# Optimization experiments

Measured on AMD Instinct MI355X. Metric: run time of the kernel, lower is better.

## Reference

```python
import jax, jax.numpy as jnp
import numpy as np


def setup_inputs() -> dict:
    key = jax.random.key(0)
    ks = jax.random.split(key, 5)
    B, S, D = 2, 2048, 1024
    x = jax.random.normal(ks[0], (B, S, D), dtype=jnp.float32)
    # nn.Linear default init scale ~ 1/sqrt(fan_in); use scaled normals
    W_qkv = jax.random.normal(ks[1], (3 * D, D), dtype=jnp.float32) * (1.0 / np.sqrt(D))
    b_qkv = jax.random.normal(ks[2], (3 * D,), dtype=jnp.float32) * 0.01
    W_out = jax.random.normal(ks[3], (D, D), dtype=jnp.float32) * (1.0 / np.sqrt(D))
    b_out = jax.random.normal(ks[4], (D,), dtype=jnp.float32) * 0.01
    return {"x": x, "W_qkv": W_qkv, "b_qkv": b_qkv, "W_out": W_out, "b_out": b_out, "n_heads": 16}


def reference(x, W_qkv, b_qkv, W_out, b_out, n_heads):
    B, S, D = x.shape
    H = n_heads
    c = D // H
    scale = jnp.asarray(1.0 / np.sqrt(c), dtype=x.dtype)
    # qkv projection; torch layout: (head, qkv, c) along the 3*D output dim
    qkv = (x @ W_qkv.T + b_qkv).reshape(B, S, H, 3, c)
    q = qkv[..., 0, :]  # (B, S, H, c)
    k = qkv[..., 1, :]
    v = qkv[..., 2, :]
    scores = jnp.einsum("bshd,bthd->bhst", q, k) * scale  # (B, H, S, S)
    # mask='right': forbid attending to future positions (col > row)
    causal = jnp.arange(S)[None, :] > jnp.arange(S)[:, None]  # (S, S) True where future
    scores = jnp.where(causal[None, None], -jnp.inf, scores)
    attn = jax.nn.softmax(scores, axis=-1)
    ctx = jnp.einsum("bhst,bthd->bshd", attn, v).reshape(B, S, D)
    return ctx @ W_out.T + b_out
```

## Files before the change

kernel.cpp:

```cpp
#include <hip/hip_runtime.h>
#include <stdint.h>

#define B_ 2
#define S_ 2048
#define D_ 1024
#define H_ 16
#define C_ 64
#define M_ (B_*S_)
#define N1_ (3*D_)

typedef float f32x4 __attribute__((ext_vector_type(4)));
typedef float f32x16 __attribute__((ext_vector_type(16)));
typedef __bf16 bf16x8 __attribute__((ext_vector_type(8)));

#define QSCALE 0.18033688f

static __device__ __forceinline__ unsigned short f2bf(float f) {
  __bf16 h = (__bf16)f;
  return __builtin_bit_cast(unsigned short, h);
}
static __device__ __forceinline__ unsigned pk2(float lo, float hi) {
  return (unsigned)f2bf(lo) | ((unsigned)f2bf(hi) << 16);
}

static __device__ __forceinline__ f32x4 mfma_bf16(uint4 a, uint4 b, f32x4 c) {
  return __builtin_amdgcn_mfma_f32_16x16x32_bf16(
      __builtin_bit_cast(bf16x8, a), __builtin_bit_cast(bf16x8, b), c, 0, 0, 0);
}
static __device__ __forceinline__ f32x16 mfma32(uint4 a, uint4 b, f32x16 c) {
  return __builtin_amdgcn_mfma_f32_32x32x16_bf16(
      __builtin_bit_cast(bf16x8, a), __builtin_bit_cast(bf16x8, b), c, 0, 0, 0);
}

static __device__ __forceinline__ float xsum32(float x) {
  return x + __shfl_xor(x, 32);
}

static __device__ __forceinline__ void gload16(const void* g, void* l) {
  __builtin_amdgcn_global_load_lds(
      (const __attribute__((address_space(1))) unsigned int*)g,
      (__attribute__((address_space(3))) unsigned int*)l, 16, 0, 0);
}

#define N8X (M_*D_/8)
#define N8W (N1_*D_/8)
#define N8O (D_*D_/8)
__global__ __launch_bounds__(256) void cast_all(
    const float* __restrict__ x,   unsigned short* __restrict__ xb,
    const float* __restrict__ wq,  unsigned short* __restrict__ wqb,
    const float* __restrict__ wo,  unsigned short* __restrict__ wob) {
  int i = blockIdx.x * 256 + threadIdx.x;
  const float* src; unsigned short* dst; int j;
  if (i < N8X)              { src = x;  dst = xb;  j = i; }
  else if (i < N8X + N8W)   { src = wq; dst = wqb; j = i - N8X; }
  else                      { src = wo; dst = wob; j = i - N8X - N8W; }
  const float4* s4 = (const float4*)src;
  float4 a = s4[2*j], b = s4[2*j+1];
  uint4 o;
  o.x = pk2(a.x, a.y);
  o.y = pk2(a.z, a.w);
  o.z = pk2(b.x, b.y);
  o.w = pk2(b.z, b.w);
  ((uint4*)dst)[j] = o;
}

template<int MODE>
__global__ __launch_bounds__(256) void gemm_bt(
    const unsigned short* __restrict__ A,
    const unsigned short* __restrict__ Bm,
    const float* __restrict__ bias,
    float* __restrict__ Cf,
    unsigned short* __restrict__ Qg,
    unsigned short* __restrict__ Kf,
    unsigned short* __restrict__ Vf,
    int Ndim, int Kdim)
{
  __shared__ __attribute__((aligned(16))) unsigned short As[128*64];
  __shared__ __attribute__((aligned(16))) unsigned short Bs[128*64];
  const int tid = threadIdx.x;
  const int l = tid & 63, wid = tid >> 6;
  const int g = l >> 4, lr = l & 15;
  const int m0 = blockIdx.y * 128, n0 = blockIdx.x * 128;
  const int wr = (wid >> 1) * 64, wc = (wid & 1) * 64;

  f32x4 acc[4][4] = {};

  const int srow8 = l >> 3;
  const int schunk = (l & 7) ^ srow8;
  const unsigned short* Agl = A + (size_t)(m0 + wid*32 + srow8) * Kdim + schunk*8;
  const unsigned short* Bgl = Bm + (size_t)(n0 + wid*32 + srow8) * Kdim + schunk*8;
  unsigned short* Adst = &As[(wid*32)*64];
  unsigned short* Bdst = &Bs[(wid*32)*64];
  const size_t rstep = (size_t)8 * Kdim;

  for (int k0 = 0; k0 < Kdim; k0 += 64) {
    __syncthreads();
#pragma unroll
    for (int i = 0; i < 4; ++i) {
      gload16(Agl + k0 + i*rstep, Adst + i*8*64);
      gload16(Bgl + k0 + i*rstep, Bdst + i*8*64);
    }
    __syncthreads();
#pragma unroll
    for (int kk = 0; kk < 2; ++kk) {
      const int c = kk*4 + g;
      uint4 af[4], bf[4];
#pragma unroll
      for (int mi = 0; mi < 4; ++mi)
        af[mi] = *(const uint4*)&As[(wr + mi*16 + lr)*64 + ((c ^ (lr & 7))*8)];
#pragma unroll
      for (int ni = 0; ni < 4; ++ni)
        bf[ni] = *(const uint4*)&Bs[(wc + ni*16 + lr)*64 + ((c ^ (lr & 7))*8)];
#pragma unroll
      for (int mi = 0; mi < 4; ++mi)
#pragma unroll
        for (int ni = 0; ni < 4; ++ni)
          acc[mi][ni] = mfma_bf16(af[mi], bf[ni], acc[mi][ni]);
    }
  }

#pragma unroll
  for (int mi = 0; mi < 4; ++mi)
#pragma unroll
    for (int ni = 0; ni < 4; ++ni) {
      if (MODE == 0) {
#pragma unroll
        for (int r = 0; r < 4; ++r) {
          const int row = m0 + wr + mi*16 + g*4 + r;
          const int col = n0 + wc + ni*16 + lr;
          Cf[(size_t)row * Ndim + col] = acc[mi][ni][r] + bias[col];
        }
      } else {
        const int colbase = n0 + wc + ni*16;
        const int h     = colbase / 192;
        const int rem   = colbase % 192;
        const int which = rem >> 6;
        const int cb    = rem & 63;
        const float bv  = bias[colbase + lr];
        const int row0  = m0 + wr + mi*16 + g*4;
        const int b     = row0 >> 11, s0 = row0 & 2047;
        const size_t bh32 = (size_t)(b*H_ + h) * 32;
        if (which == 0) {
#pragma unroll
          for (int r = 0; r < 4; ++r) {
            const float v = (acc[mi][ni][r] + bv) * QSCALE;
            Qg[((size_t)(b*H_ + h)*S_ + (s0 + r))*C_ + cb + lr] = f2bf(v);
          }
        } else if (which == 1) {
          const int kc = cb >> 4, hi = lr >> 3, j = lr & 7;
          const int kvb = s0 >> 6, kq = s0 & 63;
          const int half = kq >> 5, qlb = kq & 31;
          const size_t base = (((bh32 + kvb)*2 + half)*4 + kc)*512 + hi*256 + j;
#pragma unroll
          for (int r = 0; r < 4; ++r)
            Kf[base + (size_t)(qlb + r)*8] = f2bf(acc[mi][ni][r] + bv);
        } else {
          const int d = cb + lr;
          const int dhalf = d >> 5, ql = d & 31;
          const int kvb = s0 >> 6, kq = s0 & 63;
          const int kc = kq >> 4, hi = (kq >> 3) & 1, j0 = kq & 7;
          const size_t base = (((bh32 + kvb)*2 + dhalf)*4 + kc)*512
                              + (hi*32 + ql)*8 + j0;
          ushort4 pk;
          pk.x = f2bf(acc[mi][ni][0] + bv);
          pk.y = f2bf(acc[mi][ni][1] + bv);
          pk.z = f2bf(acc[mi][ni][2] + bv);
          pk.w = f2bf(acc[mi][ni][3] + bv);
          *(ushort4*)(Vf + base) = pk;
        }
      }
    }
}

#define PS_ 72
__global__ __launch_bounds__(256) void attn_fwd(
    const unsigned short* __restrict__ Qg,
    const unsigned short* __restrict__ Kf,
    const unsigned short* __restrict__ Vf,
    unsigned short* __restrict__ ctx)
{
  __shared__ __attribute__((aligned(16))) unsigned short Ps[4][32*PS_];
  float* Cmb0 = (float*)&Ps[0][0];
  float* Cmb1 = Cmb0 + 2112;

  const int tid = threadIdx.x, l = tid & 63, w = tid >> 6;
  const int ql = l & 31, hi = l >> 5;
  const int bh = blockIdx.x;
  const int qt = 63 - (int)blockIdx.y;
  const int qw0 = qt * 32;
  const int qg = qw0 + ql;
  const size_t baseK = (size_t)bh * S_ * C_;

  uint4 qreg[4];
  {
    const unsigned short* qp = Qg + baseK + (size_t)qg * C_ + hi * 8;
#pragma unroll
    for (int kc = 0; kc < 4; ++kc) qreg[kc] = *(const uint4*)(qp + 16*kc);
  }

  f32x16 acc0 = {}, acc1 = {};
  float lsum = 0.f;

  const unsigned short* pK = Kf + (size_t)bh * (32*4096) + (size_t)l * 8;
  const unsigned short* pV = Vf + (size_t)bh * (32*4096) + (size_t)l * 8;
  unsigned short* Pw = Ps[w];

  const int n_t = (qt + 2) >> 1;
  for (int i = w; i < n_t; i += 4) {
    const int kv0 = i * 64;
    const size_t kb = (size_t)i * 4096;

    uint4 kf0[4], kf1[4];
#pragma unroll
    for (int kc = 0; kc < 4; ++kc) {
      kf0[kc] = *(const uint4*)(pK + kb + kc*512);
      kf1[kc] = *(const uint4*)(pK + kb + 2048 + kc*512);
    }
    f32x16 st0 = {}, st1 = {};
    __builtin_amdgcn_s_setprio(1);
#pragma unroll
    for (int kc = 0; kc < 4; ++kc) {
      st0 = mfma32(kf0[kc], qreg[kc], st0);
      st1 = mfma32(kf1[kc], qreg[kc], st1);
    }
    __builtin_amdgcn_s_setprio(0);

    uint4 vf0[4], vf1[4];
#pragma unroll
    for (int kc = 0; kc < 4; ++kc) {
      vf0[kc] = *(const uint4*)(pV + kb + kc*512);
      vf1[kc] = *(const uint4*)(pV + kb + 2048 + kc*512);
    }

    if (kv0 + 63 > qw0) {
#pragma unroll
      for (int r = 0; r < 16; ++r) {
        const int krow = (r & 3) + 8*(r >> 2) + 4*hi;
        if (kv0 + krow      > qg) st0[r] = -1e30f;
        if (kv0 + 32 + krow > qg) st1[r] = -1e30f;
      }
    }

    float ps[8];
#pragma unroll
    for (int j = 0; j < 8; ++j) {
      st0[2*j]   = exp2f(st0[2*j]);
      st0[2*j+1] = exp2f(st0[2*j+1]);
      st1[2*j]   = exp2f(st1[2*j]);
      st1[2*j+1] = exp2f(st1[2*j+1]);
      ps[j] = (st0[2*j] + st0[2*j+1]) + (st1[2*j] + st1[2*j+1]);
    }
    ps[0] += ps[4]; ps[1] += ps[5]; ps[2] += ps[6]; ps[3] += ps[7];
    lsum += (ps[0] + ps[1]) + (ps[2] + ps[3]);

#pragma unroll
    for (int r = 0; r < 16; r += 4) {
      const int k0i = (r >> 2)*8 + 4*hi;
      uint2 a0, a1;
      a0.x = pk2(st0[r],   st0[r+1]);  a0.y = pk2(st0[r+2], st0[r+3]);
      a1.x = pk2(st1[r],   st1[r+1]);  a1.y = pk2(st1[r+2], st1[r+3]);
      *(uint2*)&Pw[ql*PS_ + k0i]      = a0;
      *(uint2*)&Pw[ql*PS_ + 32 + k0i] = a1;
    }
    uint4 pb[4];
#pragma unroll
    for (int kc = 0; kc < 4; ++kc)
      pb[kc] = *(const uint4*)&Pw[ql*PS_ + kc*16 + hi*8];

    __builtin_amdgcn_s_setprio(1);
#pragma unroll
    for (int kc = 0; kc < 4; ++kc) {
      acc0 = mfma32(vf0[kc], pb[kc], acc0);
      acc1 = mfma32(vf1[kc], pb[kc], acc1);
    }
    __builtin_amdgcn_s_setprio(0);
  }

  __syncthreads();
  if (w >= 2) {
    float* Cb = (w == 2) ? Cmb0 : Cmb1;
#pragma unroll
    for (int r = 0; r < 16; ++r) {
      const int d0 = (r & 3) + 8*(r >> 2) + 4*hi;
      Cb[d0*32 + ql]        = acc0[r];
      Cb[(d0 + 32)*32 + ql] = acc1[r];
    }
    Cb[2048 + l] = lsum;
  }
  __syncthreads();
  if (w < 2) {
    const float* Cb = (w == 0) ? Cmb0 : Cmb1;
#pragma unroll
    for (int r = 0; r < 16; ++r) {
      const int d0 = (r & 3) + 8*(r >> 2) + 4*hi;
      acc0[r] += Cb[d0*32 + ql];
      acc1[r] += Cb[(d0 + 32)*32 + ql];
    }
    lsum += Cb[2048 + l];
  }
  __syncthreads();
  if (w == 1) {
    float* Cb = Cmb0;
#pragma unroll
    for (int r = 0; r < 16; ++r) {
      const int d0 = (r & 3) + 8*(r >> 2) + 4*hi;
      Cb[d0*32 + ql]        = acc0[r];
      Cb[(d0 + 32)*32 + ql] = acc1[r];
    }
    Cb[2048 + l] = lsum;
  }
  __syncthreads();
  if (w != 0) return;
  {
    const float* Cb = Cmb0;
#pragma unroll
    for (int r = 0; r < 16; ++r) {
      const int d0 = (r & 3) + 8*(r >> 2) + 4*hi;
      acc0[r] += Cb[d0*32 + ql];
      acc1[r] += Cb[(d0 + 32)*32 + ql];
    }
    lsum += Cb[2048 + l];
  }

  const float inv = 1.0f / xsum32(lsum);
#pragma unroll
  for (int r = 0; r < 16; ++r) {
    const int d0 = (r & 3) + 8*(r >> 2) + 4*hi;
    Pw[ql*PS_ + ( d0       ^ (8*(ql & 7)))] = f2bf(acc0[r] * inv);
    Pw[ql*PS_ + ((32 + d0) ^ (8*(ql & 7)))] = f2bf(acc1[r] * inv);
  }
  const int q1 = l >> 1, half = l & 1;
  const unsigned short* Er = Pw + q1*PS_;
  const int b = bh >> 4, h = bh & 15;
  unsigned short* outp = ctx + ((size_t)(b*S_ + qw0 + q1))*D_ + h*C_;
#pragma unroll
  for (int j = 0; j < 4; ++j) {
    const int clog = half*4 + j;
    const int cx = clog ^ (q1 & 7);
    uint4 val = *(const uint4*)&Er[cx*8];
    *(uint4*)(outp + clog*8) = val;
  }
}

extern "C" void kernel_launch(void* const* d_in, const int* in_sizes, int n_in,
                              void* d_out, int out_size, void* d_ws, size_t ws_size,
                              hipStream_t stream) {
  const float* x    = (const float*)d_in[0];
  const float* Wqkv = (const float*)d_in[1];
  const float* bqkv = (const float*)d_in[2];
  const float* Wout = (const float*)d_in[3];
  const float* bout = (const float*)d_in[4];
  float* out = (float*)d_out;

  unsigned short* ws = (unsigned short*)d_ws;
  unsigned short* xb    = ws;
  unsigned short* wqkvb = xb    + (size_t)M_ * D_;
  unsigned short* woutb = wqkvb + (size_t)N1_ * D_;
  unsigned short* Qb    = woutb + (size_t)D_ * D_;
  unsigned short* Kfb   = Qb    + (size_t)B_*H_*S_*C_;
  unsigned short* Vfb   = Kfb   + (size_t)B_*H_*S_*C_;
  unsigned short* ctxb  = Vfb   + (size_t)B_*H_*S_*C_;

  {
    const int ntot = N8X + N8W + N8O;
    cast_all<<<dim3((ntot+255)/256), dim3(256), 0, stream>>>(
        x, xb, Wqkv, wqkvb, Wout, woutb);
  }

  gemm_bt<1><<<dim3(N1_/128, M_/128), dim3(256), 0, stream>>>(
      xb, wqkvb, bqkv, nullptr, Qb, Kfb, Vfb, N1_, D_);

  attn_fwd<<<dim3(32, 64), dim3(256), 0, stream>>>(Qb, Kfb, Vfb, ctxb);

  gemm_bt<0><<<dim3(D_/128, M_/128), dim3(256), 0, stream>>>(
      ctxb, woutb, bout, out, nullptr, nullptr, nullptr, D_, D_);
}
```

Baseline: 122.5 us.

## Double-buffer LDS tiles in GEMM to overlap global loads with MFMA

```diff
diff --git a/kernel.cpp b/kernel.cpp
--- a/kernel.cpp
+++ b/kernel.cpp
@@ -75,8 +75,8 @@
     unsigned short* __restrict__ Vf,
     int Ndim, int Kdim)
 {
-  __shared__ __attribute__((aligned(16))) unsigned short As[128*64];
-  __shared__ __attribute__((aligned(16))) unsigned short Bs[128*64];
+  __shared__ __attribute__((aligned(16))) unsigned short As[2][128*64];
+  __shared__ __attribute__((aligned(16))) unsigned short Bs[2][128*64];
   const int tid = threadIdx.x;
   const int l = tid & 63, wid = tid >> 6;
   const int g = l >> 4, lr = l & 15;
@@ -89,35 +89,45 @@
   const int schunk = (l & 7) ^ srow8;
   const unsigned short* Agl = A + (size_t)(m0 + wid*32 + srow8) * Kdim + schunk*8;
   const unsigned short* Bgl = Bm + (size_t)(n0 + wid*32 + srow8) * Kdim + schunk*8;
-  unsigned short* Adst = &As[(wid*32)*64];
-  unsigned short* Bdst = &Bs[(wid*32)*64];
+  const int doff = (wid*32)*64;
   const size_t rstep = (size_t)8 * Kdim;
 
+#define GSTAGE(BI, K0) do {                                        \
+    _Pragma("unroll")                                              \
+    for (int i_ = 0; i_ < 4; ++i_) {                               \
+      gload16(Agl + (K0) + i_*rstep, &As[BI][doff + i_*8*64]);     \
+      gload16(Bgl + (K0) + i_*rstep, &Bs[BI][doff + i_*8*64]);     \
+    }                                                              \
+  } while (0)
+
+  GSTAGE(0, 0);
+  __syncthreads();
+
+  int cur = 0;
   for (int k0 = 0; k0 < Kdim; k0 += 64) {
-    __syncthreads();
-#pragma unroll
-    for (int i = 0; i < 4; ++i) {
-      gload16(Agl + k0 + i*rstep, Adst + i*8*64);
-      gload16(Bgl + k0 + i*rstep, Bdst + i*8*64);
-    }
-    __syncthreads();
+    if (k0 + 64 < Kdim) GSTAGE(cur ^ 1, k0 + 64);
+    const unsigned short* Ab = As[cur];
+    const unsigned short* Bb = Bs[cur];
 #pragma unroll
     for (int kk = 0; kk < 2; ++kk) {
       const int c = kk*4 + g;
       uint4 af[4], bf[4];
 #pragma unroll
       for (int mi = 0; mi < 4; ++mi)
-        af[mi] = *(const uint4*)&As[(wr + mi*16 + lr)*64 + ((c ^ (lr & 7))*8)];
+        af[mi] = *(const uint4*)&Ab[(wr + mi*16 + lr)*64 + ((c ^ (lr & 7))*8)];
 #pragma unroll
       for (int ni = 0; ni < 4; ++ni)
-        bf[ni] = *(const uint4*)&Bs[(wc + ni*16 + lr)*64 + ((c ^ (lr & 7))*8)];
+        bf[ni] = *(const uint4*)&Bb[(wc + ni*16 + lr)*64 + ((c ^ (lr & 7))*8)];
 #pragma unroll
       for (int mi = 0; mi < 4; ++mi)
 #pragma unroll
         for (int ni = 0; ni < 4; ++ni)
           acc[mi][ni] = mfma_bf16(af[mi], bf[ni], acc[mi][ni]);
     }
-  }
+    __syncthreads();
+    cur ^= 1;
+  }
+#undef GSTAGE
 
 #pragma unroll
   for (int mi = 0; mi < 4; ++mi)
```

Result: faster. 118.5 us (median of 3 runs) (-3.3%).
